# Optimization experiments

Measured on AMD Instinct MI355X. Metric: run time of the kernel, lower is better.

The kernel has to match this reference:

```python
import jax, jax.numpy as jnp
import numpy as np

B, NPG, T, F, H, C, O = 16, 256, 8, 64, 64, 32, 64
N = B * NPG
E = 65536
EPS = 1e-15

def setup_inputs():
    key = jax.random.key(0)
    ks = jax.random.split(key, 12)
    pos = jax.random.normal(ks[0], (N, T, F), jnp.float32)
    g = jax.random.randint(ks[1], (E,), 0, B)
    src = g * NPG + jax.random.randint(ks[2], (E,), 0, NPG)
    dst = g * NPG + jax.random.randint(ks[3], (E,), 0, NPG)
    edge_index = jnp.stack([src, dst])
    edge_attr = jax.random.uniform(ks[4], (E,), jnp.float32)
    batch = jnp.repeat(jnp.arange(B), NPG)
    w = lambda k, s: jax.random.normal(k, s, jnp.float32) * 0.05
    return dict(
        pos=pos, edge_index=edge_index, edge_attr=edge_attr, batch=batch,
        W1=w(ks[5], (F, H)), b1=jnp.zeros((H,), jnp.float32),
        p1W=w(ks[6], (H, 2 * C)), p1b=jnp.zeros((2 * C,), jnp.float32),
        c2rW=w(ks[7], (H, H)), c2rb=jnp.zeros((H,), jnp.float32),
        c2sW=w(ks[8], (H, H)),
        p2W=w(ks[9], (H, C)), p2b=jnp.zeros((C,), jnp.float32),
        c3rW=w(ks[10], (H, O)), c3rb=jnp.zeros((O,), jnp.float32),
        c3sW=w(ks[11], (H, O)),
    )

def _gcn_conv(x, row, col, ew, W, b):
    # GCNConv with edge weights: add self loops (w=1), symmetric norm, x@W, scatter-add.
    loop = jnp.arange(N)
    r = jnp.concatenate([row, loop])
    c = jnp.concatenate([col, loop])
    w = jnp.concatenate([ew, jnp.ones((N,), ew.dtype)])
    deg = jax.ops.segment_sum(w, c, num_segments=N)
    dinv = jnp.where(deg > 0, jax.lax.rsqrt(jnp.where(deg > 0, deg, 1.0)), 0.0)
    norm = dinv[r] * w * dinv[c]
    xw = x @ W  # [N,T,H]
    out = jax.ops.segment_sum(xw[r] * norm[:, None, None], c, num_segments=N)
    return out + b

def _dense_graph_conv(x, adj, Wr, br, Ws):
    # DenseGraphConv(aggr='add'): lin_rel(adj @ x) + lin_root(x)
    return jnp.einsum('bnm,btmh->btnh', adj, x) @ Wr + br + x @ Ws

def _mincut_pool(x, adj, s, mask=None):
    # x [B,T,n,H], adj [B,n,n], s logits [B,n,k]
    s = jax.nn.softmax(s, axis=-1)
    if mask is not None:
        m = mask.astype(x.dtype)
        x = x * m[:, None, :, None]
        s = s * m[:, :, None]
    out = jnp.einsum('bnk,btnh->btkh', s, x)
    out_adj = jnp.einsum('bnk,bnm,bmj->bkj', s, adj, s)
    mincut_num = jnp.trace(out_adj, axis1=1, axis2=2)
    d_flat = adj.sum(axis=-1)  # degree vector
    mincut_den = jnp.einsum('bnk,bn,bnk->b', s, d_flat, s)  # trace(S^T D S)
    mincut_loss = jnp.mean(-(mincut_num / mincut_den))
    k = s.shape[-1]
    ss = jnp.einsum('bnk,bnj->bkj', s, s)
    ss_fro = jnp.sqrt(jnp.sum(ss * ss, axis=(1, 2), keepdims=True))
    tgt = jnp.eye(k, dtype=x.dtype) / jnp.sqrt(jnp.asarray(k, x.dtype))
    ortho_loss = jnp.mean(jnp.sqrt(jnp.sum((ss / ss_fro - tgt) ** 2, axis=(1, 2))))
    ind = jnp.arange(k)
    out_adj = out_adj.at[:, ind, ind].set(0.0)
    d = jnp.sqrt(out_adj.sum(axis=-1))[:, None] + EPS  # [B,1,k]
    out_adj = (out_adj / d) / jnp.swapaxes(d, 1, 2)
    return out, out_adj, mincut_loss, ortho_loss

def _forward(pos, edge_attr, W1, b1, p1W, p1b, c2rW, c2rb, c2sW, p2W, p2b, c3rW, c3rb, c3sW, edge_index, batch):
    row, col = edge_index[0], edge_index[1]
    h = jax.nn.relu(_gcn_conv(pos, row, col, edge_attr, W1, b1))  # [N,T,H]
    # to_dense_batch / to_dense_adj
    counts = jax.ops.segment_sum(jnp.ones((N,), jnp.int32), batch, num_segments=B)
    offsets = jnp.cumsum(counts) - counts
    pin = jnp.arange(N) - offsets[batch]  # index within graph
    xd = jnp.zeros((B, NPG, T, H), h.dtype).at[batch, pin].set(h)
    mask = jnp.zeros((B, NPG), bool).at[batch, pin].set(True)
    adj = jnp.zeros((B, NPG, NPG), h.dtype).at[batch[row], pin[row], pin[col]].add(1.0)
    x = jnp.swapaxes(xd, 1, 2)  # [B,T,n,H]
    s1 = jnp.tanh((x @ p1W + p1b).mean(axis=1))  # [B,n,2C]
    x, adj, mc1, o1 = _mincut_pool(x, adj, s1, mask)
    x = jax.nn.relu(_dense_graph_conv(x, adj, c2rW, c2rb, c2sW))  # [B,T,2C,H]
    s2 = jnp.tanh((x @ p2W + p2b).mean(axis=1))  # [B,2C,C]
    x, adj, mc2, o2 = _mincut_pool(x, adj, s2, None)
    x = _dense_graph_conv(x, adj, c3rW, c3rb, c3sW)  # [B,T,C,O]
    agg = jnp.einsum('bnc,bck->bnk', jax.nn.softmax(s1, axis=-1), jax.nn.softmax(s2, axis=-1))
    return x, mc1 + mc2, o1 + o2, agg

def reference(pos, edge_index, edge_attr, batch, W1, b1, p1W, p1b, c2rW, c2rb, c2sW, p2W, p2b, c3rW, c3rb, c3sW):
    return _forward(pos, edge_attr, W1, b1, p1W, p1b, c2rW, c2rb, c2sW, p2W, p2b, c3rW, c3rb, c3sW, edge_index, batch)
```

## Files before the change

### kernel.cpp

```cpp
#include <hip/hip_runtime.h>
#include <cstdint>


#define WS_WADJT 0
#define WS_ADN   1048576
#define WS_XW    2097152
#define WS_H     4194304
#define WS_DINV  6291456
#define WS_S1    6295552
#define WS_TMP   6557696
#define WS_DFLAT 6819840
#define WS_ADJ1  6823936
#define WS_X1    6889472
#define WS_X2    7413760
#define WS_X3    7938048
#define WS_S2    8200192
#define WS_ADJ2  8232960
#define WS_SCAL  8249344

__device__ __forceinline__ void fma4(float4& a, float s, const float4& v) {
  a.x += s * v.x; a.y += s * v.y; a.z += s * v.z; a.w += s * v.w;
}

__device__ __forceinline__ float blockRedSum4(float v, float* red) {
  #pragma unroll
  for (int m = 32; m; m >>= 1) v += __shfl_xor(v, m);
  __syncthreads();
  if ((threadIdx.x & 63) == 0) red[threadIdx.x >> 6] = v;
  __syncthreads();
  return red[0] + red[1] + red[2] + red[3];
}

__device__ __forceinline__ float blockRedSum16(float v, float* red) {
  #pragma unroll
  for (int m = 32; m; m >>= 1) v += __shfl_xor(v, m);
  __syncthreads();
  if ((threadIdx.x & 63) == 0) red[threadIdx.x >> 6] = v;
  __syncthreads();
  float s = 0.f;
  #pragma unroll
  for (int i = 0; i < 16; ++i) s += red[i];
  __syncthreads();
  return s;
}

__global__ __launch_bounds__(256) void k_p0(const float* __restrict__ pos,
                                            const float* __restrict__ W1,
                                            const int* __restrict__ ei,
                                            const float* __restrict__ ea,
                                            float* __restrict__ ws) {
  int tid = threadIdx.x, blk = blockIdx.x;
  __shared__ float sB[4096];
  if (blk < 8192) {
    for (int i = tid; i < 4096; i += 256) sB[i] = W1[i];
    __syncthreads();
    int row = blk * 4 + (tid >> 6), col = tid & 63;
    const float* a = pos + (size_t)row * 64;
    float acc = 0.f;
    #pragma unroll 8
    for (int k = 0; k < 64; ++k) acc += a[k] * sB[k * 64 + col];
    ws[WS_XW + (size_t)row * 64 + col] = acc;
  } else {
    int e = (blk - 8192) * 256 + tid;
    int s = ei[e], d = ei[65536 + e];
    int g = s >> 8, r = s & 255, c = d & 255;
    atomicAdd(&ws[WS_WADJT + (((g << 8) + c) << 8) + r], ea[e]);
    atomicAdd(&ws[WS_ADN + (((g << 8) + r) << 8) + c], 1.0f);
  }
}

__global__ __launch_bounds__(256) void k_dinv(float* __restrict__ ws) {
  int n = blockIdx.x * 4 + (threadIdx.x >> 6);
  int lane = threadIdx.x & 63;
  const float* row = ws + WS_WADJT + (size_t)n * 256;
  float s = row[lane] + row[64 + lane] + row[128 + lane] + row[192 + lane];
  #pragma unroll
  for (int m = 32; m; m >>= 1) s += __shfl_xor(s, m);
  if (lane == 0) ws[WS_DINV + n] = rsqrtf(s + 1.0f);
}

__global__ __launch_bounds__(256) void k_gcn_s1(float* __restrict__ ws,
                                                const float* __restrict__ b1,
                                                const float* __restrict__ p1W,
                                                const float* __restrict__ p1b) {
  __shared__ float pL[256];
  __shared__ int iL[256];
  __shared__ int wcnt[4];
  __shared__ float red4[256];
  __shared__ float xm[64];
  int n = blockIdx.x;
  int g = n >> 8, cc = n & 255;
  int tid = threadIdx.x;
  int w = tid >> 6, lane = tid & 63;
  const float* dinv = ws + WS_DINV;
  float dn = dinv[n];
  float pv = ws[WS_WADJT + (size_t)n * 256 + tid] * dinv[(g << 8) + tid] * dn;
  if (tid == cc) pv += dn * dn;
  bool act = (pv != 0.f);
  unsigned long long mask = __ballot(act);
  int wpos = (int)__popcll(mask & ((1ull << lane) - 1ull));
  if (lane == 0) wcnt[w] = (int)__popcll(mask);
  __syncthreads();
  int base = 0;
  #pragma unroll
  for (int i = 0; i < 4; ++i) base += (i < w) ? wcnt[i] : 0;
  int na = wcnt[0] + wcnt[1] + wcnt[2] + wcnt[3];
  if (act) { iL[base + wpos] = tid; pL[base + wpos] = pv; }
  __syncthreads();
  const float* xg = ws + WS_XW + (size_t)g * 131072;
  float acc0 = 0.f, acc1 = 0.f;
  for (int i = 0; i < na; ++i) {
    int r = iL[i];
    float p = pL[i];
    acc0 += p * xg[(size_t)r * 512 + tid];
    acc1 += p * xg[(size_t)r * 512 + 256 + tid];
  }
  float bb = b1[tid & 63];
  acc0 = fmaxf(acc0 + bb, 0.f);
  acc1 = fmaxf(acc1 + bb, 0.f);
  float* hp = ws + WS_H + (size_t)n * 512;
  hp[tid] = acc0;
  hp[256 + tid] = acc1;
  red4[w * 64 + (tid & 63)] = acc0 + acc1;
  __syncthreads();
  if (tid < 64) {
    xm[tid] = 0.125f * (red4[tid] + red4[64 + tid] + red4[128 + tid] + red4[192 + tid]);
    float a = p1b[tid];
    #pragma unroll 4
    for (int k = 0; k < 64; ++k) a += xm[k] * p1W[k * 64 + tid];
    float v = tanhf(a);
    float mx = v;
    #pragma unroll
    for (int m = 32; m; m >>= 1) mx = fmaxf(mx, __shfl_xor(mx, m));
    float e = __expf(v - mx);
    float se = e;
    #pragma unroll
    for (int m = 32; m; m >>= 1) se += __shfl_xor(se, m);
    ws[WS_S1 + (size_t)n * 64 + tid] = e / se;
  }
}

__global__ __launch_bounds__(256) void k_as1_x1(float* __restrict__ ws) {
  __shared__ float smem[4096];
  int tid = threadIdx.x, blk = blockIdx.x;
  if (blk < 1024) {
    int* iL = (int*)smem;
    float* aL = smem + 1024;
    int w = tid >> 6, lane = tid & 63;
    int n = blk * 4 + w, g = n >> 8;
    float4 av = *(const float4*)(ws + WS_ADN + (size_t)n * 256 + lane * 4);
    float rs = av.x + av.y + av.z + av.w;
    #pragma unroll
    for (int m = 32; m; m >>= 1) rs += __shfl_xor(rs, m);
    if (lane == 0) ws[WS_DFLAT + n] = rs;
    float avv[4] = {av.x, av.y, av.z, av.w};
    unsigned long long below = (1ull << lane) - 1ull;
    int base = 0;
    #pragma unroll
    for (int q = 0; q < 4; ++q) {
      bool act = (avv[q] != 0.f);
      unsigned long long mask = __ballot(act);
      if (act) {
        int pos = base + (int)__popcll(mask & below);
        iL[w * 256 + pos] = lane * 4 + q;
        aL[w * 256 + pos] = avv[q];
      }
      base += (int)__popcll(mask);
    }
    int na = base;
    float acc = 0.f;
    const float* S1g = ws + WS_S1 + ((size_t)g << 8) * 64;
    for (int i = 0; i < na; ++i) {
      int m = iL[w * 256 + i];
      float a = aL[w * 256 + i];
      acc += a * S1g[(size_t)m * 64 + lane];
    }
    ws[WS_TMP + (size_t)n * 64 + lane] = acc;
  } else {
    int bt = blk - 1024;
    int b = bt >> 3, t = bt & 7;
    int hc = tid & 63, kb = (tid >> 6) * 16;
    float* sS = smem;
    float* sX = smem + 2048;
    float acc[16];
    #pragma unroll
    for (int q = 0; q < 16; ++q) acc[q] = 0.f;
    for (int n0 = 0; n0 < 256; n0 += 32) {
      __syncthreads();
      for (int idx = tid; idx < 2048; idx += 256) {
        int i = idx >> 6, c = idx & 63;
        sS[idx] = ws[WS_S1 + ((size_t)((b << 8) + n0 + i)) * 64 + c];
        sX[idx] = ws[WS_H + ((size_t)((b << 8) + n0 + i)) * 512 + t * 64 + c];
      }
      __syncthreads();
      for (int i = 0; i < 32; ++i) {
        float xv = sX[i * 64 + hc];
        #pragma unroll
        for (int q = 0; q < 16; ++q) acc[q] += sS[i * 64 + kb + q] * xv;
      }
    }
    #pragma unroll
    for (int q = 0; q < 16; ++q)
      ws[WS_X1 + ((size_t)bt * 64 + kb + q) * 64 + hc] = acc[q];
  }
}

__global__ __launch_bounds__(1024) void k_pool1(float* __restrict__ ws) {
  __shared__ float S1c[2048];
  __shared__ float Tc[2048];
  __shared__ float prs[1088];
  __shared__ float diagL[64];
  __shared__ float dd[64];
  __shared__ float red[16];
  int b = blockIdx.x, tid = threadIdx.x;
  int k = tid >> 4, j0 = (tid & 15) * 4;
  const float* Sb = ws + WS_S1 + (size_t)b * 16384;
  const float* Tb = ws + WS_TMP + (size_t)b * 16384;
  float accA[4] = {0, 0, 0, 0}, accS[4] = {0, 0, 0, 0};
  for (int n0 = 0; n0 < 256; n0 += 32) {
    __syncthreads();
    S1c[tid] = Sb[n0 * 64 + tid];
    S1c[tid + 1024] = Sb[n0 * 64 + 1024 + tid];
    Tc[tid] = Tb[n0 * 64 + tid];
    Tc[tid + 1024] = Tb[n0 * 64 + 1024 + tid];
    __syncthreads();
    for (int i = 0; i < 32; ++i) {
      float sk = S1c[i * 64 + k];
      float4 tv = *(const float4*)(Tc + i * 64 + j0);
      float4 sv = *(const float4*)(S1c + i * 64 + j0);
      fma4(*(float4*)accA, sk, tv);
      fma4(*(float4*)accS, sk, sv);
    }
  }
  float num = 0.f, fro2 = 0.f, rsp = 0.f;
  #pragma unroll
  for (int q = 0; q < 4; ++q) { rsp += accA[q]; fro2 += accS[q] * accS[q]; }
  if (k >= j0 && k < j0 + 4) { num = accA[k - j0]; diagL[k] = accA[k - j0]; }
  prs[k * 17 + (tid & 15)] = rsp;
  __syncthreads();
  if (tid < 64) {
    float rs = 0.f;
    #pragma unroll
    for (int i = 0; i < 16; ++i) rs += prs[tid * 17 + i];
    dd[tid] = sqrtf(fmaxf(rs - diagL[tid], 0.f)) + 1e-15f;
  }
  float denp = 0.f;
  if (tid < 256) {
    const float* s = Sb + tid * 64;
    float q = 0.f;
    for (int kk = 0; kk < 64; kk += 4) {
      float4 v = *(const float4*)(s + kk);
      q += v.x * v.x + v.y * v.y + v.z * v.z + v.w * v.w;
    }
    denp = q * ws[WS_DFLAT + (b << 8) + tid];
  }
  float numT = blockRedSum16(num, red);
  float denT = blockRedSum16(denp, red);
  float froT = sqrtf(blockRedSum16(fro2, red));
  float inv_fro = 1.f / froT;
  float osum = 0.f;
  #pragma unroll
  for (int q = 0; q < 4; ++q) {
    float v = accS[q] * inv_fro - ((j0 + q) == k ? 0.125f : 0.f);
    osum += v * v;
  }
  float orT = blockRedSum16(osum, red);
  float* adj = ws + WS_ADJ1 + (size_t)b * 4096;
  float dk = dd[k];
  #pragma unroll
  for (int q = 0; q < 4; ++q) {
    int j = j0 + q;
    adj[k * 64 + j] = (k == j) ? 0.f : accA[q] / (dk * dd[j]);
  }
  if (tid == 0) {
    ws[WS_SCAL + b] = numT / denT;
    ws[WS_SCAL + 16 + b] = sqrtf(orT);
  }
}

__global__ __launch_bounds__(256) void k_conv2(float* __restrict__ ws,
                                               const float* __restrict__ Wr,
                                               const float* __restrict__ br,
                                               const float* __restrict__ Ws) {
  int bt = blockIdx.x;
  int b = bt >> 3;
  int tid = threadIdx.x;
  __shared__ float sA[64 * 65];
  __shared__ float sX[64 * 65];
  __shared__ float sY[64 * 65];
  __shared__ float sWr[64 * 65];
  __shared__ float sWs[64 * 65];
  for (int idx = tid; idx < 4096; idx += 256) {
    int r = idx >> 6, c = idx & 63;
    sA[r * 65 + c] = ws[WS_ADJ1 + (size_t)b * 4096 + idx];
    sX[r * 65 + c] = ws[WS_X1 + (size_t)bt * 4096 + idx];
    sWr[r * 65 + c] = Wr[idx];
    sWs[r * 65 + c] = Ws[idx];
  }
  __syncthreads();
  int n = tid >> 2, h0 = (tid & 3) * 16;
  float acc[16];
  #pragma unroll
  for (int q = 0; q < 16; ++q) acc[q] = 0.f;
  for (int m = 0; m < 64; ++m) {
    float a = sA[n * 65 + m];
    #pragma unroll
    for (int q = 0; q < 16; ++q) acc[q] += a * sX[m * 65 + h0 + q];
  }
  #pragma unroll
  for (int q = 0; q < 16; ++q) sY[n * 65 + h0 + q] = acc[q];
  __syncthreads();
  #pragma unroll
  for (int q = 0; q < 16; ++q) acc[q] = br[h0 + q];
  for (int m = 0; m < 64; ++m) {
    float y = sY[n * 65 + m], x = sX[n * 65 + m];
    #pragma unroll
    for (int q = 0; q < 16; ++q)
      acc[q] += y * sWr[m * 65 + h0 + q] + x * sWs[m * 65 + h0 + q];
  }
  #pragma unroll
  for (int q = 0; q < 16; ++q)
    ws[WS_X2 + (size_t)bt * 4096 + n * 64 + h0 + q] = fmaxf(acc[q], 0.f);
}

__global__ __launch_bounds__(64) void k_s2(float* __restrict__ ws,
                                           const float* __restrict__ p2W,
                                           const float* __restrict__ p2b) {
  int bn = blockIdx.x;
  int b = bn >> 6, n = bn & 63;
  int f = threadIdx.x;
  __shared__ float xm[64];
  float s = 0.f;
  #pragma unroll
  for (int t = 0; t < 8; ++t) s += ws[WS_X2 + ((size_t)(b * 8 + t) * 64 + n) * 64 + f];
  xm[f] = s * 0.125f;
  __syncthreads();
  if (f < 32) {
    float acc = p2b[f];
    #pragma unroll 4
    for (int k = 0; k < 64; ++k) acc += xm[k] * p2W[k * 32 + f];
    float v = tanhf(acc);
    float m = v;
    #pragma unroll
    for (int off = 16; off; off >>= 1) m = fmaxf(m, __shfl_xor(m, off, 32));
    float e = __expf(v - m);
    float sum = e;
    #pragma unroll
    for (int off = 16; off; off >>= 1) sum += __shfl_xor(sum, off, 32);
    ws[WS_S2 + (size_t)(b * 64 + n) * 32 + f] = e / sum;
  }
}

__global__ __launch_bounds__(256) void k_x3_pool2(float* __restrict__ ws) {
  __shared__ float sm[10700];
  int tid = threadIdx.x, blk = blockIdx.x;
  if (blk < 128) {
    int bt = blk, b = bt >> 3;
    float* sX = sm;
    float* sS = sm + 4160;
    for (int idx = tid; idx < 4096; idx += 256)
      sX[(idx >> 6) * 65 + (idx & 63)] = ws[WS_X2 + (size_t)bt * 4096 + idx];
    for (int idx = tid; idx < 2048; idx += 256)
      sS[(idx >> 5) * 33 + (idx & 31)] = ws[WS_S2 + (size_t)b * 2048 + idx];
    __syncthreads();
    int k = tid >> 3, h0 = (tid & 7) * 8;
    float acc[8];
    #pragma unroll
    for (int q = 0; q < 8; ++q) acc[q] = 0.f;
    for (int n = 0; n < 64; ++n) {
      float sv = sS[n * 33 + k];
      #pragma unroll
      for (int q = 0; q < 8; ++q) acc[q] += sv * sX[n * 65 + h0 + q];
    }
    #pragma unroll
    for (int q = 0; q < 8; ++q)
      ws[WS_X3 + (size_t)bt * 2048 + k * 64 + h0 + q] = acc[q];
  } else {
    int b = blk - 128;
    float* sA = sm;
    float* sS2 = sm + 4160;
    float* sT = sm + 6272;
    float* oaL = sm + 8384;
    float* ssL = sm + 9440;
    float* sdf = sm + 10496;
    float* ddL = sm + 10560;
    float* red = sm + 10592;
    for (int idx = tid; idx < 4096; idx += 256)
      sA[(idx >> 6) * 65 + (idx & 63)] = ws[WS_ADJ1 + (size_t)b * 4096 + idx];
    for (int idx = tid; idx < 2048; idx += 256)
      sS2[(idx >> 5) * 33 + (idx & 31)] = ws[WS_S2 + (size_t)b * 2048 + idx];
    __syncthreads();
    if (tid < 64) {
      float s = 0.f;
      for (int m = 0; m < 64; ++m) s += sA[tid * 65 + m];
      sdf[tid] = s;
    }
    {
      int n = tid >> 2, j0 = (tid & 3) * 8;
      float acc[8];
      #pragma unroll
      for (int q = 0; q < 8; ++q) acc[q] = 0.f;
      for (int m = 0; m < 64; ++m) {
        float a = sA[n * 65 + m];
        #pragma unroll
        for (int q = 0; q < 8; ++q) acc[q] += a * sS2[m * 33 + j0 + q];
      }
      #pragma unroll
      for (int q = 0; q < 8; ++q) sT[n * 33 + j0 + q] = acc[q];
    }
    float accD = 0.f;
    if (tid < 64) {
      float t = 0.f;
      for (int q = 0; q < 32; ++q) { float v = sS2[tid * 33 + q]; t += v * v; }
      accD = t;
    }
    __syncthreads();
    if (tid < 64) accD *= sdf[tid];
    int k = tid >> 3, j0 = (tid & 7) * 4;
    float accA[4], accS[4];
    #pragma unroll
    for (int q = 0; q < 4; ++q) { accA[q] = 0.f; accS[q] = 0.f; }
    for (int n = 0; n < 64; ++n) {
      float sk = sS2[n * 33 + k];
      #pragma unroll
      for (int q = 0; q < 4; ++q) {
        accA[q] += sk * sT[n * 33 + j0 + q];
        accS[q] += sk * sS2[n * 33 + j0 + q];
      }
    }
    #pragma unroll
    for (int q = 0; q < 4; ++q) {
      oaL[k * 33 + j0 + q] = accA[q];
      ssL[k * 33 + j0 + q] = accS[q];
    }
    float fro2p = 0.f;
    #pragma unroll
    for (int q = 0; q < 4; ++q) fro2p += accS[q] * accS[q];
    __syncthreads();
    float num = 0.f, trs = 0.f;
    if (tid < 32) {
      num = oaL[tid * 33 + tid];
      trs = ssL[tid * 33 + tid];
      float rs = 0.f;
      for (int j = 0; j < 32; ++j) rs += oaL[tid * 33 + j];
      ddL[tid] = sqrtf(fmaxf(rs - num, 0.f)) + 1e-15f;
    }
    float numT = blockRedSum4(num, red);
    float denT = blockRedSum4(accD, red);
    float froT = sqrtf(blockRedSum4(fro2p, red));
    float trT = blockRedSum4(trs, red);
    __syncthreads();
    {
      int idx = tid * 4, kk = idx >> 5, jj = idx & 31;
      float dk = ddL[kk];
      float* a2 = ws + WS_ADJ2 + (size_t)b * 1024;
      #pragma unroll
      for (int q = 0; q < 4; ++q) {
        int j = jj + q;
        a2[kk * 32 + j] = (kk == j) ? 0.f : oaL[kk * 33 + j] / (dk * ddL[j]);
      }
    }
    if (tid == 0) {
      ws[WS_SCAL + 32 + b] = numT / denT;
      ws[WS_SCAL + 48 + b] = sqrtf(fmaxf(2.f - 2.f * trT / (5.656854249f * froT), 0.f));
    }
  }
}

__global__ __launch_bounds__(256) void k_final(float* __restrict__ ws,
                                               const float* __restrict__ Wr,
                                               const float* __restrict__ br,
                                               const float* __restrict__ Ws,
                                               float* __restrict__ out) {
  __shared__ float sm[13600];
  int tid = threadIdx.x, blk = blockIdx.x;
  if (blk < 128) {
    int bt = blk, b = bt >> 3;
    float* sX = sm;
    float* sA = sm + 2080;
    float* sY = sm + 3136;
    float* sWr = sm + 5216;
    float* sWs = sm + 9376;
    for (int idx = tid; idx < 2048; idx += 256)
      sX[(idx >> 6) * 65 + (idx & 63)] = ws[WS_X3 + (size_t)bt * 2048 + idx];
    for (int idx = tid; idx < 1024; idx += 256)
      sA[(idx >> 5) * 33 + (idx & 31)] = ws[WS_ADJ2 + (size_t)b * 1024 + idx];
    for (int idx = tid; idx < 4096; idx += 256) {
      int r = idx >> 6, c = idx & 63;
      sWr[r * 65 + c] = Wr[idx];
      sWs[r * 65 + c] = Ws[idx];
    }
    __syncthreads();
    int n = tid >> 3, h0 = (tid & 7) * 8;
    float acc[8];
    #pragma unroll
    for (int q = 0; q < 8; ++q) acc[q] = 0.f;
    for (int m = 0; m < 32; ++m) {
      float a = sA[n * 33 + m];
      #pragma unroll
      for (int q = 0; q < 8; ++q) acc[q] += a * sX[m * 65 + h0 + q];
    }
    #pragma unroll
    for (int q = 0; q < 8; ++q) sY[n * 65 + h0 + q] = acc[q];
    __syncthreads();
    #pragma unroll
    for (int q = 0; q < 8; ++q) acc[q] = br[h0 + q];
    for (int m = 0; m < 64; ++m) {
      float y = sY[n * 65 + m], x = sX[n * 65 + m];
      #pragma unroll
      for (int q = 0; q < 8; ++q)
        acc[q] += y * sWr[m * 65 + h0 + q] + x * sWs[m * 65 + h0 + q];
    }
    #pragma unroll
    for (int q = 0; q < 8; ++q) out[(size_t)bt * 2048 + n * 64 + h0 + q] = acc[q];
  } else if (blk < 640) {
    int bi = blk - 128;
    int b = bi >> 5;
    int n0 = (bi & 31) * 8;
    float* sS = sm;
    for (int idx = tid; idx < 2048; idx += 256)
      sS[(idx >> 5) * 33 + (idx & 31)] = ws[WS_S2 + (size_t)b * 2048 + idx];
    __syncthreads();
    int n = n0 + (tid >> 5), j = tid & 31;
    const float* s1r = ws + WS_S1 + ((size_t)((b << 8) + n)) * 64;
    float acc = 0.f;
    #pragma unroll 4
    for (int k = 0; k < 64; ++k) acc += s1r[k] * sS[k * 33 + j];
    out[262146 + ((size_t)((b << 8) + n)) * 32 + j] = acc;
  } else if (tid == 0) {
    float mc = 0.f, o = 0.f;
    #pragma unroll
    for (int b2 = 0; b2 < 16; ++b2) {
      mc += ws[WS_SCAL + b2] + ws[WS_SCAL + 32 + b2];
      o += ws[WS_SCAL + 16 + b2] + ws[WS_SCAL + 48 + b2];
    }
    out[262144] = -mc / 16.0f;
    out[262145] = o / 16.0f;
  }
}

extern "C" void kernel_launch(void* const* d_in, const int* in_sizes, int n_in,
                              void* d_out, int out_size, void* d_ws, size_t ws_size,
                              hipStream_t stream) {
  (void)in_sizes; (void)n_in; (void)out_size; (void)ws_size;
  const float* pos = (const float*)d_in[0];
  const int* ei = (const int*)d_in[1];
  const float* ea = (const float*)d_in[2];
  const float* W1 = (const float*)d_in[4];
  const float* b1 = (const float*)d_in[5];
  const float* p1W = (const float*)d_in[6];
  const float* p1b = (const float*)d_in[7];
  const float* c2rW = (const float*)d_in[8];
  const float* c2rb = (const float*)d_in[9];
  const float* c2sW = (const float*)d_in[10];
  const float* p2W = (const float*)d_in[11];
  const float* p2b = (const float*)d_in[12];
  const float* c3rW = (const float*)d_in[13];
  const float* c3rb = (const float*)d_in[14];
  const float* c3sW = (const float*)d_in[15];
  float* ws = (float*)d_ws;
  float* out = (float*)d_out;

  hipMemsetAsync(d_ws, 0, (size_t)2097152 * sizeof(float), stream);
  k_p0<<<dim3(8448), dim3(256), 0, stream>>>(pos, W1, ei, ea, ws);
  k_dinv<<<dim3(1024), dim3(256), 0, stream>>>(ws);
  k_gcn_s1<<<dim3(4096), dim3(256), 0, stream>>>(ws, b1, p1W, p1b);
  k_as1_x1<<<dim3(1152), dim3(256), 0, stream>>>(ws);
  k_pool1<<<dim3(16), dim3(1024), 0, stream>>>(ws);
  k_conv2<<<dim3(128), dim3(256), 0, stream>>>(ws, c2rW, c2rb, c2sW);
  k_s2<<<dim3(1024), dim3(64), 0, stream>>>(ws, p2W, p2b);
  k_x3_pool2<<<dim3(144), dim3(256), 0, stream>>>(ws);
  k_final<<<dim3(641), dim3(256), 0, stream>>>(ws, c3rW, c3rb, c3sW, out);
}
```

Baseline: 264.0 us.

## Fuse all stages into one persistent kernel with software grid barriers

Replaces the memset and nine separate kernel launches with one persistent 256-block kernel whose stages are separated by an atomic-counter grid barrier. Workspace zeroing moves inside the kernel. Degree sums are accumulated with atomics during edge scatter, which removes the separate dinv pass. Pool1 now runs with 256 threads instead of 1024 and overlaps with the x1 computation. This cuts launch overhead and inter-kernel gaps, but much larger stages now run on only 256 blocks, which lowers parallelism. It also relies on all blocks being co-resident for the spin barrier to work.

```diff
diff --git a/kernel.cpp b/kernel.cpp
--- a/kernel.cpp
+++ b/kernel.cpp
@@ -4,9 +4,9 @@
 
 #define WS_WADJT 0
 #define WS_ADN   1048576
-#define WS_XW    2097152
-#define WS_H     4194304
-#define WS_DINV  6291456
+#define WS_WSUM  2097152
+#define WS_XW    2101248
+#define WS_H     4198400
 #define WS_S1    6295552
 #define WS_TMP   6557696
 #define WS_DFLAT 6819840
@@ -17,9 +17,25 @@
 #define WS_S2    8200192
 #define WS_ADJ2  8232960
 #define WS_SCAL  8249344
-
-__device__ __forceinline__ void fma4(float4& a, float s, const float4& v) {
-  a.x += s * v.x; a.y += s * v.y; a.z += s * v.z; a.w += s * v.w;
+#define WS_BAR   8249408
+
+#define NBLK 256
+
+__device__ __forceinline__ void gridBarrier(int* cnt, int* gen) {
+  __syncthreads();
+  if (threadIdx.x == 0) {
+    __threadfence();
+    int g = __hip_atomic_load(gen, __ATOMIC_RELAXED, __HIP_MEMORY_SCOPE_AGENT);
+    int a = __hip_atomic_fetch_add(cnt, 1, __ATOMIC_ACQ_REL, __HIP_MEMORY_SCOPE_AGENT);
+    if (a == NBLK - 1) {
+      __hip_atomic_store(cnt, 0, __ATOMIC_RELAXED, __HIP_MEMORY_SCOPE_AGENT);
+      __hip_atomic_fetch_add(gen, 1, __ATOMIC_ACQ_REL, __HIP_MEMORY_SCOPE_AGENT);
+    } else {
+      while (__hip_atomic_load(gen, __ATOMIC_RELAXED, __HIP_MEMORY_SCOPE_AGENT) == g) {}
+    }
+    __threadfence();
+  }
+  __syncthreads();
 }
 
 __device__ __forceinline__ float blockRedSum4(float v, float* red) {
@@ -31,157 +47,236 @@
   return red[0] + red[1] + red[2] + red[3];
 }
 
-__device__ __forceinline__ float blockRedSum16(float v, float* red) {
-  #pragma unroll
-  for (int m = 32; m; m >>= 1) v += __shfl_xor(v, m);
-  __syncthreads();
-  if ((threadIdx.x & 63) == 0) red[threadIdx.x >> 6] = v;
-  __syncthreads();
-  float s = 0.f;
-  #pragma unroll
-  for (int i = 0; i < 16; ++i) s += red[i];
-  __syncthreads();
-  return s;
-}
-
-__global__ __launch_bounds__(256) void k_p0(const float* __restrict__ pos,
-                                            const float* __restrict__ W1,
-                                            const int* __restrict__ ei,
-                                            const float* __restrict__ ea,
-                                            float* __restrict__ ws) {
+__global__ __launch_bounds__(256) void k_mega(
+    const float* __restrict__ pos, const int* __restrict__ ei, const float* __restrict__ ea,
+    const float* __restrict__ W1, const float* __restrict__ b1,
+    const float* __restrict__ p1W, const float* __restrict__ p1b,
+    const float* __restrict__ c2rW, const float* __restrict__ c2rb, const float* __restrict__ c2sW,
+    const float* __restrict__ p2W, const float* __restrict__ p2b,
+    const float* __restrict__ c3rW, const float* __restrict__ c3rb, const float* __restrict__ c3sW,
+    float* __restrict__ ws, float* __restrict__ out)
+{
+  int* bcnt = (int*)(ws + WS_BAR);
+  int* bgen = (int*)(ws + WS_BAR) + 1;
+  __shared__ float sm[20800];
   int tid = threadIdx.x, blk = blockIdx.x;
-  __shared__ float sB[4096];
-  if (blk < 8192) {
-    for (int i = tid; i < 4096; i += 256) sB[i] = W1[i];
-    __syncthreads();
-    int row = blk * 4 + (tid >> 6), col = tid & 63;
-    const float* a = pos + (size_t)row * 64;
-    float acc = 0.f;
-    #pragma unroll 8
-    for (int k = 0; k < 64; ++k) acc += a[k] * sB[k * 64 + col];
-    ws[WS_XW + (size_t)row * 64 + col] = acc;
-  } else {
-    int e = (blk - 8192) * 256 + tid;
+  int gtid = blk * 256 + tid;
+
+  {
+    float4* p = (float4*)ws;
+    for (int i = gtid; i < 525312; i += 65536) p[i] = make_float4(0.f, 0.f, 0.f, 0.f);
+  }
+  gridBarrier(bcnt, bgen);
+
+  {
+    for (int i = tid; i < 4096; i += 256) sm[i] = W1[i];
+    __syncthreads();
+    int col = tid & 63;
+    for (int pass = 0; pass < 32; ++pass) {
+      int row = blk * 128 + pass * 4 + (tid >> 6);
+      const float* a = pos + (size_t)row * 64;
+      float acc = 0.f;
+      #pragma unroll 8
+      for (int k = 0; k < 64; ++k) acc += a[k] * sm[k * 64 + col];
+      ws[WS_XW + (size_t)row * 64 + col] = acc;
+    }
+    int e = gtid;
     int s = ei[e], d = ei[65536 + e];
     int g = s >> 8, r = s & 255, c = d & 255;
-    atomicAdd(&ws[WS_WADJT + (((g << 8) + c) << 8) + r], ea[e]);
-    atomicAdd(&ws[WS_ADN + (((g << 8) + r) << 8) + c], 1.0f);
-  }
-}
-
-__global__ __launch_bounds__(256) void k_dinv(float* __restrict__ ws) {
-  int n = blockIdx.x * 4 + (threadIdx.x >> 6);
-  int lane = threadIdx.x & 63;
-  const float* row = ws + WS_WADJT + (size_t)n * 256;
-  float s = row[lane] + row[64 + lane] + row[128 + lane] + row[192 + lane];
-  #pragma unroll
-  for (int m = 32; m; m >>= 1) s += __shfl_xor(s, m);
-  if (lane == 0) ws[WS_DINV + n] = rsqrtf(s + 1.0f);
-}
-
-__global__ __launch_bounds__(256) void k_gcn_s1(float* __restrict__ ws,
-                                                const float* __restrict__ b1,
-                                                const float* __restrict__ p1W,
-                                                const float* __restrict__ p1b) {
-  __shared__ float pL[256];
-  __shared__ int iL[256];
-  __shared__ int wcnt[4];
-  __shared__ float red4[256];
-  __shared__ float xm[64];
-  int n = blockIdx.x;
-  int g = n >> 8, cc = n & 255;
-  int tid = threadIdx.x;
-  int w = tid >> 6, lane = tid & 63;
-  const float* dinv = ws + WS_DINV;
-  float dn = dinv[n];
-  float pv = ws[WS_WADJT + (size_t)n * 256 + tid] * dinv[(g << 8) + tid] * dn;
-  if (tid == cc) pv += dn * dn;
-  bool act = (pv != 0.f);
-  unsigned long long mask = __ballot(act);
-  int wpos = (int)__popcll(mask & ((1ull << lane) - 1ull));
-  if (lane == 0) wcnt[w] = (int)__popcll(mask);
-  __syncthreads();
-  int base = 0;
-  #pragma unroll
-  for (int i = 0; i < 4; ++i) base += (i < w) ? wcnt[i] : 0;
-  int na = wcnt[0] + wcnt[1] + wcnt[2] + wcnt[3];
-  if (act) { iL[base + wpos] = tid; pL[base + wpos] = pv; }
-  __syncthreads();
-  const float* xg = ws + WS_XW + (size_t)g * 131072;
-  float acc0 = 0.f, acc1 = 0.f;
-  for (int i = 0; i < na; ++i) {
-    int r = iL[i];
-    float p = pL[i];
-    acc0 += p * xg[(size_t)r * 512 + tid];
-    acc1 += p * xg[(size_t)r * 512 + 256 + tid];
-  }
-  float bb = b1[tid & 63];
-  acc0 = fmaxf(acc0 + bb, 0.f);
-  acc1 = fmaxf(acc1 + bb, 0.f);
-  float* hp = ws + WS_H + (size_t)n * 512;
-  hp[tid] = acc0;
-  hp[256 + tid] = acc1;
-  red4[w * 64 + (tid & 63)] = acc0 + acc1;
-  __syncthreads();
-  if (tid < 64) {
-    xm[tid] = 0.125f * (red4[tid] + red4[64 + tid] + red4[128 + tid] + red4[192 + tid]);
-    float a = p1b[tid];
-    #pragma unroll 4
-    for (int k = 0; k < 64; ++k) a += xm[k] * p1W[k * 64 + tid];
-    float v = tanhf(a);
-    float mx = v;
-    #pragma unroll
-    for (int m = 32; m; m >>= 1) mx = fmaxf(mx, __shfl_xor(mx, m));
-    float e = __expf(v - mx);
-    float se = e;
-    #pragma unroll
-    for (int m = 32; m; m >>= 1) se += __shfl_xor(se, m);
-    ws[WS_S1 + (size_t)n * 64 + tid] = e / se;
-  }
-}
-
-__global__ __launch_bounds__(256) void k_as1_x1(float* __restrict__ ws) {
-  __shared__ float smem[4096];
-  int tid = threadIdx.x, blk = blockIdx.x;
-  if (blk < 1024) {
-    int* iL = (int*)smem;
-    float* aL = smem + 1024;
+    float w = ea[e];
+    atomicAdd(&ws[WS_WADJT + (size_t)(((g << 8) + c) << 8) + r], w);
+    atomicAdd(&ws[WS_ADN + (size_t)(((g << 8) + r) << 8) + c], 1.0f);
+    atomicAdd(&ws[WS_WSUM + (g << 8) + c], w);
+  }
+  gridBarrier(bcnt, bgen);
+
+  {
+    float* sW = sm;
+    float* dinvL = sm + 4096;
+    float* pL = sm + 4352;
+    float* red4 = sm + 4608;
+    float* xm = sm + 4864;
+    int* iL = (int*)(sm + 4928);
+    int* wcnt = (int*)(sm + 5184);
+    int g = blk >> 4;
+    for (int i = tid; i < 4096; i += 256) sW[i] = p1W[i];
+    dinvL[tid] = rsqrtf(ws[WS_WSUM + (g << 8) + tid] + 1.0f);
+    __syncthreads();
     int w = tid >> 6, lane = tid & 63;
-    int n = blk * 4 + w, g = n >> 8;
-    float4 av = *(const float4*)(ws + WS_ADN + (size_t)n * 256 + lane * 4);
-    float rs = av.x + av.y + av.z + av.w;
-    #pragma unroll
-    for (int m = 32; m; m >>= 1) rs += __shfl_xor(rs, m);
-    if (lane == 0) ws[WS_DFLAT + n] = rs;
-    float avv[4] = {av.x, av.y, av.z, av.w};
-    unsigned long long below = (1ull << lane) - 1ull;
-    int base = 0;
-    #pragma unroll
-    for (int q = 0; q < 4; ++q) {
-      bool act = (avv[q] != 0.f);
+    float bb = b1[tid & 63];
+    for (int it = 0; it < 16; ++it) {
+      int n = blk * 16 + it;
+      int cc = n & 255;
+      float dn = dinvL[cc];
+      float pv = ws[WS_WADJT + (size_t)n * 256 + tid] * dinvL[tid] * dn;
+      if (tid == cc) pv += dn * dn;
+      bool act = (pv != 0.f);
       unsigned long long mask = __ballot(act);
-      if (act) {
-        int pos = base + (int)__popcll(mask & below);
-        iL[w * 256 + pos] = lane * 4 + q;
-        aL[w * 256 + pos] = avv[q];
-      }
-      base += (int)__popcll(mask);
-    }
-    int na = base;
-    float acc = 0.f;
-    const float* S1g = ws + WS_S1 + ((size_t)g << 8) * 64;
-    for (int i = 0; i < na; ++i) {
-      int m = iL[w * 256 + i];
-      float a = aL[w * 256 + i];
-      acc += a * S1g[(size_t)m * 64 + lane];
-    }
-    ws[WS_TMP + (size_t)n * 64 + lane] = acc;
-  } else {
-    int bt = blk - 1024;
+      int wpos = (int)__popcll(mask & ((1ull << lane) - 1ull));
+      if (lane == 0) wcnt[w] = (int)__popcll(mask);
+      __syncthreads();
+      int base = 0;
+      #pragma unroll
+      for (int i = 0; i < 4; ++i) base += (i < w) ? wcnt[i] : 0;
+      int na = wcnt[0] + wcnt[1] + wcnt[2] + wcnt[3];
+      if (act) { iL[base + wpos] = tid; pL[base + wpos] = pv; }
+      __syncthreads();
+      const float* xg = ws + WS_XW + (size_t)g * 131072;
+      float acc0 = 0.f, acc1 = 0.f;
+      for (int i = 0; i < na; ++i) {
+        int r = iL[i];
+        float p = pL[i];
+        acc0 += p * xg[(size_t)r * 512 + tid];
+        acc1 += p * xg[(size_t)r * 512 + 256 + tid];
+      }
+      acc0 = fmaxf(acc0 + bb, 0.f);
+      acc1 = fmaxf(acc1 + bb, 0.f);
+      float* hp = ws + WS_H + (size_t)n * 512;
+      hp[tid] = acc0;
+      hp[256 + tid] = acc1;
+      red4[w * 64 + (tid & 63)] = acc0 + acc1;
+      __syncthreads();
+      if (tid < 64) {
+        xm[tid] = 0.125f * (red4[tid] + red4[64 + tid] + red4[128 + tid] + red4[192 + tid]);
+        float a = p1b[tid];
+        #pragma unroll 4
+        for (int kq = 0; kq < 64; ++kq) a += xm[kq] * sW[kq * 64 + tid];
+        float v = tanhf(a);
+        float mx = v;
+        #pragma unroll
+        for (int m = 32; m; m >>= 1) mx = fmaxf(mx, __shfl_xor(mx, m));
+        float e = __expf(v - mx);
+        float se = e;
+        #pragma unroll
+        for (int m = 32; m; m >>= 1) se += __shfl_xor(se, m);
+        ws[WS_S1 + (size_t)n * 64 + tid] = e / se;
+      }
+      __syncthreads();
+    }
+  }
+  gridBarrier(bcnt, bgen);
+
+  {
+    float* aL = sm;
+    int* iLa = (int*)(sm + 1024);
+    int w = tid >> 6, lane = tid & 63;
+    for (int nit = 0; nit < 4; ++nit) {
+      int n = nit * 1024 + blk * 4 + w;
+      int g = n >> 8;
+      float4 av = *(const float4*)(ws + WS_ADN + (size_t)n * 256 + lane * 4);
+      float rs = av.x + av.y + av.z + av.w;
+      #pragma unroll
+      for (int m = 32; m; m >>= 1) rs += __shfl_xor(rs, m);
+      if (lane == 0) ws[WS_DFLAT + n] = rs;
+      float avv[4] = {av.x, av.y, av.z, av.w};
+      unsigned long long below = (1ull << lane) - 1ull;
+      int base = 0;
+      #pragma unroll
+      for (int q = 0; q < 4; ++q) {
+        bool act = (avv[q] != 0.f);
+        unsigned long long mask = __ballot(act);
+        if (act) {
+          int p = base + (int)__popcll(mask & below);
+          iLa[w * 256 + p] = lane * 4 + q;
+          aL[w * 256 + p] = avv[q];
+        }
+        base += (int)__popcll(mask);
+      }
+      int na = base;
+      float acc = 0.f;
+      const float* S1g = ws + WS_S1 + ((size_t)g << 8) * 64;
+      for (int i = 0; i < na; ++i) {
+        int m = iLa[w * 256 + i];
+        float a = aL[w * 256 + i];
+        acc += a * S1g[(size_t)m * 64 + lane];
+      }
+      ws[WS_TMP + (size_t)n * 64 + lane] = acc;
+    }
+  }
+  gridBarrier(bcnt, bgen);
+
+  if (blk < 16) {
+    int b = blk;
+    float* S1c = sm;
+    float* Tc = sm + 2048;
+    float* prs = sm + 4096;
+    float* diagL = sm + 4416;
+    float* dd = sm + 4480;
+    float* red = sm + 4544;
+    const float* Sb = ws + WS_S1 + (size_t)b * 16384;
+    const float* Tb = ws + WS_TMP + (size_t)b * 16384;
+    int k = tid >> 2, j0 = (tid & 3) * 16;
+    float accA[16], accS[16];
+    #pragma unroll
+    for (int q = 0; q < 16; ++q) { accA[q] = 0.f; accS[q] = 0.f; }
+    for (int n0 = 0; n0 < 256; n0 += 32) {
+      __syncthreads();
+      for (int i = tid; i < 2048; i += 256) { S1c[i] = Sb[n0 * 64 + i]; Tc[i] = Tb[n0 * 64 + i]; }
+      __syncthreads();
+      for (int i = 0; i < 32; ++i) {
+        float sk = S1c[i * 64 + k];
+        const float4* tp = (const float4*)(Tc + i * 64 + j0);
+        const float4* sp = (const float4*)(S1c + i * 64 + j0);
+        #pragma unroll
+        for (int q4 = 0; q4 < 4; ++q4) {
+          float4 tv = tp[q4], sv = sp[q4];
+          accA[q4 * 4 + 0] += sk * tv.x; accA[q4 * 4 + 1] += sk * tv.y;
+          accA[q4 * 4 + 2] += sk * tv.z; accA[q4 * 4 + 3] += sk * tv.w;
+          accS[q4 * 4 + 0] += sk * sv.x; accS[q4 * 4 + 1] += sk * sv.y;
+          accS[q4 * 4 + 2] += sk * sv.z; accS[q4 * 4 + 3] += sk * sv.w;
+        }
+      }
+    }
+    float num = 0.f, fro2 = 0.f, rsp = 0.f;
+    #pragma unroll
+    for (int q = 0; q < 16; ++q) { rsp += accA[q]; fro2 += accS[q] * accS[q]; }
+    #pragma unroll
+    for (int q = 0; q < 16; ++q)
+      if (j0 + q == k) { num = accA[q]; diagL[k] = accA[q]; }
+    prs[k * 5 + (tid & 3)] = rsp;
+    __syncthreads();
+    if (tid < 64) {
+      float rs = prs[tid * 5] + prs[tid * 5 + 1] + prs[tid * 5 + 2] + prs[tid * 5 + 3];
+      dd[tid] = sqrtf(fmaxf(rs - diagL[tid], 0.f)) + 1e-15f;
+    }
+    float denp;
+    {
+      const float* s = Sb + tid * 64;
+      float qq = 0.f;
+      for (int kk = 0; kk < 64; kk += 4) {
+        float4 v = *(const float4*)(s + kk);
+        qq += v.x * v.x + v.y * v.y + v.z * v.z + v.w * v.w;
+      }
+      denp = qq * ws[WS_DFLAT + (b << 8) + tid];
+    }
+    float numT = blockRedSum4(num, red);
+    float denT = blockRedSum4(denp, red);
+    float froT = sqrtf(blockRedSum4(fro2, red));
+    float inv_fro = 1.f / froT;
+    float osum = 0.f;
+    #pragma unroll
+    for (int q = 0; q < 16; ++q) {
+      float v = accS[q] * inv_fro - ((j0 + q) == k ? 0.125f : 0.f);
+      osum += v * v;
+    }
+    float orT = blockRedSum4(osum, red);
+    float* adj = ws + WS_ADJ1 + (size_t)b * 4096;
+    float dk = dd[k];
+    #pragma unroll
+    for (int q = 0; q < 16; ++q) {
+      int j = j0 + q;
+      adj[k * 64 + j] = (k == j) ? 0.f : accA[q] / (dk * dd[j]);
+    }
+    if (tid == 0) {
+      ws[WS_SCAL + b] = numT / denT;
+      ws[WS_SCAL + 16 + b] = sqrtf(orT);
+    }
+  } else if (blk >= 64 && blk < 192) {
+    int bt = blk - 64;
     int b = bt >> 3, t = bt & 7;
     int hc = tid & 63, kb = (tid >> 6) * 16;
-    float* sS = smem;
-    float* sX = smem + 2048;
+    float* sS = sm;
+    float* sX = sm + 2048;
     float acc[16];
     #pragma unroll
     for (int q = 0; q < 16; ++q) acc[q] = 0.f;
@@ -203,157 +298,181 @@
     for (int q = 0; q < 16; ++q)
       ws[WS_X1 + ((size_t)bt * 64 + kb + q) * 64 + hc] = acc[q];
   }
-}
-
-__global__ __launch_bounds__(1024) void k_pool1(float* __restrict__ ws) {
-  __shared__ float S1c[2048];
-  __shared__ float Tc[2048];
-  __shared__ float prs[1088];
-  __shared__ float diagL[64];
-  __shared__ float dd[64];
-  __shared__ float red[16];
-  int b = blockIdx.x, tid = threadIdx.x;
-  int k = tid >> 4, j0 = (tid & 15) * 4;
-  const float* Sb = ws + WS_S1 + (size_t)b * 16384;
-  const float* Tb = ws + WS_TMP + (size_t)b * 16384;
-  float accA[4] = {0, 0, 0, 0}, accS[4] = {0, 0, 0, 0};
-  for (int n0 = 0; n0 < 256; n0 += 32) {
-    __syncthreads();
-    S1c[tid] = Sb[n0 * 64 + tid];
-    S1c[tid + 1024] = Sb[n0 * 64 + 1024 + tid];
-    Tc[tid] = Tb[n0 * 64 + tid];
-    Tc[tid + 1024] = Tb[n0 * 64 + 1024 + tid];
-    __syncthreads();
-    for (int i = 0; i < 32; ++i) {
-      float sk = S1c[i * 64 + k];
-      float4 tv = *(const float4*)(Tc + i * 64 + j0);
-      float4 sv = *(const float4*)(S1c + i * 64 + j0);
-      fma4(*(float4*)accA, sk, tv);
-      fma4(*(float4*)accS, sk, sv);
-    }
-  }
-  float num = 0.f, fro2 = 0.f, rsp = 0.f;
-  #pragma unroll
-  for (int q = 0; q < 4; ++q) { rsp += accA[q]; fro2 += accS[q] * accS[q]; }
-  if (k >= j0 && k < j0 + 4) { num = accA[k - j0]; diagL[k] = accA[k - j0]; }
-  prs[k * 17 + (tid & 15)] = rsp;
-  __syncthreads();
-  if (tid < 64) {
-    float rs = 0.f;
-    #pragma unroll
-    for (int i = 0; i < 16; ++i) rs += prs[tid * 17 + i];
-    dd[tid] = sqrtf(fmaxf(rs - diagL[tid], 0.f)) + 1e-15f;
-  }
-  float denp = 0.f;
-  if (tid < 256) {
-    const float* s = Sb + tid * 64;
-    float q = 0.f;
-    for (int kk = 0; kk < 64; kk += 4) {
-      float4 v = *(const float4*)(s + kk);
-      q += v.x * v.x + v.y * v.y + v.z * v.z + v.w * v.w;
-    }
-    denp = q * ws[WS_DFLAT + (b << 8) + tid];
-  }
-  float numT = blockRedSum16(num, red);
-  float denT = blockRedSum16(denp, red);
-  float froT = sqrtf(blockRedSum16(fro2, red));
-  float inv_fro = 1.f / froT;
-  float osum = 0.f;
-  #pragma unroll
-  for (int q = 0; q < 4; ++q) {
-    float v = accS[q] * inv_fro - ((j0 + q) == k ? 0.125f : 0.f);
-    osum += v * v;
-  }
-  float orT = blockRedSum16(osum, red);
-  float* adj = ws + WS_ADJ1 + (size_t)b * 4096;
-  float dk = dd[k];
-  #pragma unroll
-  for (int q = 0; q < 4; ++q) {
-    int j = j0 + q;
-    adj[k * 64 + j] = (k == j) ? 0.f : accA[q] / (dk * dd[j]);
-  }
-  if (tid == 0) {
-    ws[WS_SCAL + b] = numT / denT;
-    ws[WS_SCAL + 16 + b] = sqrtf(orT);
-  }
-}
-
-__global__ __launch_bounds__(256) void k_conv2(float* __restrict__ ws,
-                                               const float* __restrict__ Wr,
-                                               const float* __restrict__ br,
-                                               const float* __restrict__ Ws) {
-  int bt = blockIdx.x;
-  int b = bt >> 3;
-  int tid = threadIdx.x;
-  __shared__ float sA[64 * 65];
-  __shared__ float sX[64 * 65];
-  __shared__ float sY[64 * 65];
-  __shared__ float sWr[64 * 65];
-  __shared__ float sWs[64 * 65];
-  for (int idx = tid; idx < 4096; idx += 256) {
-    int r = idx >> 6, c = idx & 63;
-    sA[r * 65 + c] = ws[WS_ADJ1 + (size_t)b * 4096 + idx];
-    sX[r * 65 + c] = ws[WS_X1 + (size_t)bt * 4096 + idx];
-    sWr[r * 65 + c] = Wr[idx];
-    sWs[r * 65 + c] = Ws[idx];
-  }
-  __syncthreads();
-  int n = tid >> 2, h0 = (tid & 3) * 16;
-  float acc[16];
-  #pragma unroll
-  for (int q = 0; q < 16; ++q) acc[q] = 0.f;
-  for (int m = 0; m < 64; ++m) {
-    float a = sA[n * 65 + m];
-    #pragma unroll
-    for (int q = 0; q < 16; ++q) acc[q] += a * sX[m * 65 + h0 + q];
-  }
-  #pragma unroll
-  for (int q = 0; q < 16; ++q) sY[n * 65 + h0 + q] = acc[q];
-  __syncthreads();
-  #pragma unroll
-  for (int q = 0; q < 16; ++q) acc[q] = br[h0 + q];
-  for (int m = 0; m < 64; ++m) {
-    float y = sY[n * 65 + m], x = sX[n * 65 + m];
+  gridBarrier(bcnt, bgen);
+
+  if (blk < 128) {
+    int bt = blk;
+    int b = bt >> 3;
+    float* sA = sm;
+    float* sX = sm + 4160;
+    float* sY = sm + 8320;
+    float* sWr = sm + 12480;
+    float* sWs = sm + 16640;
+    for (int idx = tid; idx < 4096; idx += 256) {
+      int r = idx >> 6, c = idx & 63;
+      sA[r * 65 + c] = ws[WS_ADJ1 + (size_t)b * 4096 + idx];
+      sX[r * 65 + c] = ws[WS_X1 + (size_t)bt * 4096 + idx];
+      sWr[r * 65 + c] = c2rW[idx];
+      sWs[r * 65 + c] = c2sW[idx];
+    }
+    __syncthreads();
+    int n = tid >> 2, h0 = (tid & 3) * 16;
+    float acc[16];
+    #pragma unroll
+    for (int q = 0; q < 16; ++q) acc[q] = 0.f;
+    for (int m = 0; m < 64; ++m) {
+      float a = sA[n * 65 + m];
+      #pragma unroll
+      for (int q = 0; q < 16; ++q) acc[q] += a * sX[m * 65 + h0 + q];
+    }
+    #pragma unroll
+    for (int q = 0; q < 16; ++q) sY[n * 65 + h0 + q] = acc[q];
+    __syncthreads();
+    #pragma unroll
+    for (int q = 0; q < 16; ++q) acc[q] = c2rb[h0 + q];
+    for (int m = 0; m < 64; ++m) {
+      float y = sY[n * 65 + m], x = sX[n * 65 + m];
+      #pragma unroll
+      for (int q = 0; q < 16; ++q)
+        acc[q] += y * sWr[m * 65 + h0 + q] + x * sWs[m * 65 + h0 + q];
+    }
     #pragma unroll
     for (int q = 0; q < 16; ++q)
-      acc[q] += y * sWr[m * 65 + h0 + q] + x * sWs[m * 65 + h0 + q];
-  }
-  #pragma unroll
-  for (int q = 0; q < 16; ++q)
-    ws[WS_X2 + (size_t)bt * 4096 + n * 64 + h0 + q] = fmaxf(acc[q], 0.f);
-}
-
-__global__ __launch_bounds__(64) void k_s2(float* __restrict__ ws,
-                                           const float* __restrict__ p2W,
-                                           const float* __restrict__ p2b) {
-  int bn = blockIdx.x;
-  int b = bn >> 6, n = bn & 63;
-  int f = threadIdx.x;
-  __shared__ float xm[64];
-  float s = 0.f;
-  #pragma unroll
-  for (int t = 0; t < 8; ++t) s += ws[WS_X2 + ((size_t)(b * 8 + t) * 64 + n) * 64 + f];
-  xm[f] = s * 0.125f;
-  __syncthreads();
-  if (f < 32) {
-    float acc = p2b[f];
-    #pragma unroll 4
-    for (int k = 0; k < 64; ++k) acc += xm[k] * p2W[k * 32 + f];
-    float v = tanhf(acc);
-    float m = v;
-    #pragma unroll
-    for (int off = 16; off; off >>= 1) m = fmaxf(m, __shfl_xor(m, off, 32));
-    float e = __expf(v - m);
-    float sum = e;
-    #pragma unroll
-    for (int off = 16; off; off >>= 1) sum += __shfl_xor(sum, off, 32);
-    ws[WS_S2 + (size_t)(b * 64 + n) * 32 + f] = e / sum;
-  }
-}
-
-__global__ __launch_bounds__(256) void k_x3_pool2(float* __restrict__ ws) {
-  __shared__ float sm[10700];
-  int tid = threadIdx.x, blk = blockIdx.x;
+      ws[WS_X2 + (size_t)bt * 4096 + n * 64 + h0 + q] = fmaxf(acc[q], 0.f);
+  }
+  gridBarrier(bcnt, bgen);
+
+  if (blk < 16) {
+    int b = blk;
+    float* xmL = sm;
+    float* sS2 = sm + 4096;
+    float* sA2 = sm + 6208;
+    float* sT  = sm + 10368;
+    float* oaL = sm + 12480;
+    float* ssL = sm + 13536;
+    float* sdf = sm + 14592;
+    float* ddL = sm + 14656;
+    float* red = sm + 14688;
+    float* sp2W = sm + 14692;
+    for (int idx = tid; idx < 4096; idx += 256)
+      sA2[(idx >> 6) * 65 + (idx & 63)] = ws[WS_ADJ1 + (size_t)b * 4096 + idx];
+    for (int idx = tid; idx < 2048; idx += 256) sp2W[idx] = p2W[idx];
+    for (int idx = tid; idx < 4096; idx += 256) {
+      int n = idx >> 6, f = idx & 63;
+      float s = 0.f;
+      #pragma unroll
+      for (int t = 0; t < 8; ++t)
+        s += ws[WS_X2 + ((size_t)(b * 8 + t) * 64 + n) * 64 + f];
+      xmL[idx] = s * 0.125f;
+    }
+    __syncthreads();
+    {
+      int n = tid >> 2, jq = (tid & 3) * 8;
+      float acc[8];
+      #pragma unroll
+      for (int q = 0; q < 8; ++q) acc[q] = p2b[jq + q];
+      for (int kq = 0; kq < 64; ++kq) {
+        float v = xmL[n * 64 + kq];
+        #pragma unroll
+        for (int q = 0; q < 8; ++q) acc[q] += v * sp2W[kq * 32 + jq + q];
+      }
+      float vq[8];
+      float mx = -1e30f;
+      #pragma unroll
+      for (int q = 0; q < 8; ++q) { vq[q] = tanhf(acc[q]); mx = fmaxf(mx, vq[q]); }
+      mx = fmaxf(mx, __shfl_xor(mx, 1));
+      mx = fmaxf(mx, __shfl_xor(mx, 2));
+      float eq[8], se = 0.f;
+      #pragma unroll
+      for (int q = 0; q < 8; ++q) { eq[q] = __expf(vq[q] - mx); se += eq[q]; }
+      se += __shfl_xor(se, 1);
+      se += __shfl_xor(se, 2);
+      float inv = 1.f / se;
+      #pragma unroll
+      for (int q = 0; q < 8; ++q) {
+        float e = eq[q] * inv;
+        sS2[n * 33 + jq + q] = e;
+        ws[WS_S2 + (size_t)(b * 64 + n) * 32 + jq + q] = e;
+      }
+    }
+    __syncthreads();
+    if (tid < 64) {
+      float s = 0.f;
+      for (int m = 0; m < 64; ++m) s += sA2[tid * 65 + m];
+      sdf[tid] = s;
+    }
+    {
+      int n = tid >> 2, j0 = (tid & 3) * 8;
+      float acc[8];
+      #pragma unroll
+      for (int q = 0; q < 8; ++q) acc[q] = 0.f;
+      for (int m = 0; m < 64; ++m) {
+        float a = sA2[n * 65 + m];
+        #pragma unroll
+        for (int q = 0; q < 8; ++q) acc[q] += a * sS2[m * 33 + j0 + q];
+      }
+      #pragma unroll
+      for (int q = 0; q < 8; ++q) sT[n * 33 + j0 + q] = acc[q];
+    }
+    float accD = 0.f;
+    if (tid < 64) {
+      float t = 0.f;
+      for (int q = 0; q < 32; ++q) { float v = sS2[tid * 33 + q]; t += v * v; }
+      accD = t;
+    }
+    __syncthreads();
+    if (tid < 64) accD *= sdf[tid];
+    int k = tid >> 3, j0 = (tid & 7) * 4;
+    float accA[4], accS[4];
+    #pragma unroll
+    for (int q = 0; q < 4; ++q) { accA[q] = 0.f; accS[q] = 0.f; }
+    for (int n = 0; n < 64; ++n) {
+      float sk = sS2[n * 33 + k];
+      #pragma unroll
+      for (int q = 0; q < 4; ++q) {
+        accA[q] += sk * sT[n * 33 + j0 + q];
+        accS[q] += sk * sS2[n * 33 + j0 + q];
+      }
+    }
+    #pragma unroll
+    for (int q = 0; q < 4; ++q) {
+      oaL[k * 33 + j0 + q] = accA[q];
+      ssL[k * 33 + j0 + q] = accS[q];
+    }
+    float fro2p = 0.f;
+    #pragma unroll
+    for (int q = 0; q < 4; ++q) fro2p += accS[q] * accS[q];
+    __syncthreads();
+    float num = 0.f, trs = 0.f;
+    if (tid < 32) {
+      num = oaL[tid * 33 + tid];
+      trs = ssL[tid * 33 + tid];
+      float rs = 0.f;
+      for (int j = 0; j < 32; ++j) rs += oaL[tid * 33 + j];
+      ddL[tid] = sqrtf(fmaxf(rs - num, 0.f)) + 1e-15f;
+    }
+    float numT = blockRedSum4(num, red);
+    float denT = blockRedSum4(accD, red);
+    float froT = sqrtf(blockRedSum4(fro2p, red));
+    float trT = blockRedSum4(trs, red);
+    __syncthreads();
+    {
+      int idx = tid * 4, kk = idx >> 5, jj = idx & 31;
+      float dk = ddL[kk];
+      float* a2 = ws + WS_ADJ2 + (size_t)b * 1024;
+      #pragma unroll
+      for (int q = 0; q < 4; ++q) {
+        int j = jj + q;
+        a2[kk * 32 + j] = (kk == j) ? 0.f : oaL[kk * 33 + j] / (dk * ddL[j]);
+      }
+    }
+    if (tid == 0) {
+      ws[WS_SCAL + 32 + b] = numT / denT;
+      ws[WS_SCAL + 48 + b] = sqrtf(fmaxf(2.f - 2.f * trT / (5.656854249f * froT), 0.f));
+    }
+  }
+  gridBarrier(bcnt, bgen);
+
   if (blk < 128) {
     int bt = blk, b = bt >> 3;
     float* sX = sm;
@@ -376,104 +495,34 @@
     for (int q = 0; q < 8; ++q)
       ws[WS_X3 + (size_t)bt * 2048 + k * 64 + h0 + q] = acc[q];
   } else {
-    int b = blk - 128;
-    float* sA = sm;
-    float* sS2 = sm + 4160;
-    float* sT = sm + 6272;
-    float* oaL = sm + 8384;
-    float* ssL = sm + 9440;
-    float* sdf = sm + 10496;
-    float* ddL = sm + 10560;
-    float* red = sm + 10592;
-    for (int idx = tid; idx < 4096; idx += 256)
-      sA[(idx >> 6) * 65 + (idx & 63)] = ws[WS_ADJ1 + (size_t)b * 4096 + idx];
+    int rb = blk - 128;
+    int b = rb >> 3, sub = rb & 7;
+    float* sS = sm;
     for (int idx = tid; idx < 2048; idx += 256)
-      sS2[(idx >> 5) * 33 + (idx & 31)] = ws[WS_S2 + (size_t)b * 2048 + idx];
-    __syncthreads();
-    if (tid < 64) {
-      float s = 0.f;
-      for (int m = 0; m < 64; ++m) s += sA[tid * 65 + m];
-      sdf[tid] = s;
-    }
-    {
-      int n = tid >> 2, j0 = (tid & 3) * 8;
-      float acc[8];
-      #pragma unroll
-      for (int q = 0; q < 8; ++q) acc[q] = 0.f;
-      for (int m = 0; m < 64; ++m) {
-        float a = sA[n * 65 + m];
-        #pragma unroll
-        for (int q = 0; q < 8; ++q) acc[q] += a * sS2[m * 33 + j0 + q];
-      }
-      #pragma unroll
-      for (int q = 0; q < 8; ++q) sT[n * 33 + j0 + q] = acc[q];
-    }
-    float accD = 0.f;
-    if (tid < 64) {
-      float t = 0.f;
-      for (int q = 0; q < 32; ++q) { float v = sS2[tid * 33 + q]; t += v * v; }
-      accD = t;
-    }
-    __syncthreads();
-    if (tid < 64) accD *= sdf[tid];
-    int k = tid >> 3, j0 = (tid & 7) * 4;
-    float accA[4], accS[4];
-    #pragma unroll
-    for (int q = 0; q < 4; ++q) { accA[q] = 0.f; accS[q] = 0.f; }
-    for (int n = 0; n < 64; ++n) {
-      float sk = sS2[n * 33 + k];
-      #pragma unroll
-      for (int q = 0; q < 4; ++q) {
-        accA[q] += sk * sT[n * 33 + j0 + q];
-        accS[q] += sk * sS2[n * 33 + j0 + q];
-      }
-    }
-    #pragma unroll
-    for (int q = 0; q < 4; ++q) {
-      oaL[k * 33 + j0 + q] = accA[q];
-      ssL[k * 33 + j0 + q] = accS[q];
-    }
-    float fro2p = 0.f;
-    #pragma unroll
-    for (int q = 0; q < 4; ++q) fro2p += accS[q] * accS[q];
-    __syncthreads();
-    float num = 0.f, trs = 0.f;
-    if (tid < 32) {
-      num = oaL[tid * 33 + tid];
-      trs = ssL[tid * 33 + tid];
-      float rs = 0.f;
-      for (int j = 0; j < 32; ++j) rs += oaL[tid * 33 + j];
-      ddL[tid] = sqrtf(fmaxf(rs - num, 0.f)) + 1e-15f;
-    }
-    float numT = blockRedSum4(num, red);
-    float denT = blockRedSum4(accD, red);
-    float froT = sqrtf(blockRedSum4(fro2p, red));
-    float trT = blockRedSum4(trs, red);
-    __syncthreads();
-    {
-      int idx = tid * 4, kk = idx >> 5, jj = idx & 31;
-      float dk = ddL[kk];
-      float* a2 = ws + WS_ADJ2 + (size_t)b * 1024;
-      #pragma unroll
-      for (int q = 0; q < 4; ++q) {
-        int j = jj + q;
-        a2[kk * 32 + j] = (kk == j) ? 0.f : oaL[kk * 33 + j] / (dk * ddL[j]);
-      }
-    }
-    if (tid == 0) {
-      ws[WS_SCAL + 32 + b] = numT / denT;
-      ws[WS_SCAL + 48 + b] = sqrtf(fmaxf(2.f - 2.f * trT / (5.656854249f * froT), 0.f));
-    }
-  }
-}
-
-__global__ __launch_bounds__(256) void k_final(float* __restrict__ ws,
-                                               const float* __restrict__ Wr,
-                                               const float* __restrict__ br,
-                                               const float* __restrict__ Ws,
-                                               float* __restrict__ out) {
-  __shared__ float sm[13600];
-  int tid = threadIdx.x, blk = blockIdx.x;
+      sS[(idx >> 5) * 33 + (idx & 31)] = ws[WS_S2 + (size_t)b * 2048 + idx];
+    __syncthreads();
+    for (int jt = 0; jt < 4; ++jt) {
+      int n0 = (sub * 4 + jt) * 8;
+      int n = n0 + (tid >> 5), j = tid & 31;
+      const float* s1r = ws + WS_S1 + ((size_t)((b << 8) + n)) * 64;
+      float acc = 0.f;
+      #pragma unroll 4
+      for (int kq = 0; kq < 64; ++kq) acc += s1r[kq] * sS[kq * 33 + j];
+      out[262146 + ((size_t)((b << 8) + n)) * 32 + j] = acc;
+    }
+    if (blk == 255 && tid == 0) {
+      float mc = 0.f, o = 0.f;
+      #pragma unroll
+      for (int b2 = 0; b2 < 16; ++b2) {
+        mc += ws[WS_SCAL + b2] + ws[WS_SCAL + 32 + b2];
+        o += ws[WS_SCAL + 16 + b2] + ws[WS_SCAL + 48 + b2];
+      }
+      out[262144] = -mc / 16.0f;
+      out[262145] = o / 16.0f;
+    }
+  }
+  gridBarrier(bcnt, bgen);
+
   if (blk < 128) {
     int bt = blk, b = bt >> 3;
     float* sX = sm;
@@ -487,8 +536,8 @@
       sA[(idx >> 5) * 33 + (idx & 31)] = ws[WS_ADJ2 + (size_t)b * 1024 + idx];
     for (int idx = tid; idx < 4096; idx += 256) {
       int r = idx >> 6, c = idx & 63;
-      sWr[r * 65 + c] = Wr[idx];
-      sWs[r * 65 + c] = Ws[idx];
+      sWr[r * 65 + c] = c3rW[idx];
+      sWs[r * 65 + c] = c3sW[idx];
     }
     __syncthreads();
     int n = tid >> 3, h0 = (tid & 7) * 8;
@@ -504,7 +553,7 @@
     for (int q = 0; q < 8; ++q) sY[n * 65 + h0 + q] = acc[q];
     __syncthreads();
     #pragma unroll
-    for (int q = 0; q < 8; ++q) acc[q] = br[h0 + q];
+    for (int q = 0; q < 8; ++q) acc[q] = c3rb[h0 + q];
     for (int m = 0; m < 64; ++m) {
       float y = sY[n * 65 + m], x = sX[n * 65 + m];
       #pragma unroll
@@ -513,29 +562,6 @@
     }
     #pragma unroll
     for (int q = 0; q < 8; ++q) out[(size_t)bt * 2048 + n * 64 + h0 + q] = acc[q];
-  } else if (blk < 640) {
-    int bi = blk - 128;
-    int b = bi >> 5;
-    int n0 = (bi & 31) * 8;
-    float* sS = sm;
-    for (int idx = tid; idx < 2048; idx += 256)
-      sS[(idx >> 5) * 33 + (idx & 31)] = ws[WS_S2 + (size_t)b * 2048 + idx];
-    __syncthreads();
-    int n = n0 + (tid >> 5), j = tid & 31;
-    const float* s1r = ws + WS_S1 + ((size_t)((b << 8) + n)) * 64;
-    float acc = 0.f;
-    #pragma unroll 4
-    for (int k = 0; k < 64; ++k) acc += s1r[k] * sS[k * 33 + j];
-    out[262146 + ((size_t)((b << 8) + n)) * 32 + j] = acc;
-  } else if (tid == 0) {
-    float mc = 0.f, o = 0.f;
-    #pragma unroll
-    for (int b2 = 0; b2 < 16; ++b2) {
-      mc += ws[WS_SCAL + b2] + ws[WS_SCAL + 32 + b2];
-      o += ws[WS_SCAL + 16 + b2] + ws[WS_SCAL + 48 + b2];
-    }
-    out[262144] = -mc / 16.0f;
-    out[262145] = o / 16.0f;
   }
 }
 
@@ -561,14 +587,8 @@
   float* ws = (float*)d_ws;
   float* out = (float*)d_out;
 
-  hipMemsetAsync(d_ws, 0, (size_t)2097152 * sizeof(float), stream);
-  k_p0<<<dim3(8448), dim3(256), 0, stream>>>(pos, W1, ei, ea, ws);
-  k_dinv<<<dim3(1024), dim3(256), 0, stream>>>(ws);
-  k_gcn_s1<<<dim3(4096), dim3(256), 0, stream>>>(ws, b1, p1W, p1b);
-  k_as1_x1<<<dim3(1152), dim3(256), 0, stream>>>(ws);
-  k_pool1<<<dim3(16), dim3(1024), 0, stream>>>(ws);
-  k_conv2<<<dim3(128), dim3(256), 0, stream>>>(ws, c2rW, c2rb, c2sW);
-  k_s2<<<dim3(1024), dim3(64), 0, stream>>>(ws, p2W, p2b);
-  k_x3_pool2<<<dim3(144), dim3(256), 0, stream>>>(ws);
-  k_final<<<dim3(641), dim3(256), 0, stream>>>(ws, c3rW, c3rb, c3sW, out);
+  hipMemsetAsync((char*)d_ws + (size_t)WS_BAR * 4, 0, 8, stream);
+  k_mega<<<dim3(NBLK), dim3(256), 0, stream>>>(
+      pos, ei, ea, W1, b1, p1W, p1b, c2rW, c2rb, c2sW,
+      p2W, p2b, c3rW, c3rb, c3sW, ws, out);
 }
```

After: 530.2 us. 101% more time.
